# Performance work log

Measured on AMD Instinct MI355X. Metric: run time of the kernel, lower is better.

The kernel has to match this reference:

```python
import jax, jax.numpy as jnp
import numpy as np

F6_E3M2_MAX = 28.0  # max representable e3m2 value
M_TOKENS, K_IN, N_OUT = 256, 4096, 4096


def _quantize_e3m2(w: np.ndarray) -> np.ndarray:
    """Round-to-nearest onto the FP6 e3m2 grid (bias=3, min normal 2^-2, subnormal step 2^-4)."""
    sign = np.sign(w)
    a = np.minimum(np.abs(w), F6_E3M2_MAX)
    e = np.clip(np.floor(np.log2(np.maximum(a, 1e-30))), -2.0, 4.0)
    step = np.exp2(e - 2.0)  # 2 mantissa bits -> 4 steps per octave; subnormal step = 2^-4
    q = np.round(a / step) * step
    return (sign * np.minimum(q, F6_E3M2_MAX)).astype(np.float32)


def setup_inputs() -> dict:
    key = jax.random.key(0)
    k_x, k_w, k_b = jax.random.split(key, 3)
    x = (jax.random.normal(k_x, (M_TOKENS, K_IN), dtype=jnp.float32)).astype(jnp.float16)
    w_fp32 = np.asarray(jax.random.normal(k_w, (N_OUT, K_IN), dtype=jnp.float32)) * 0.02
    # per-row scale as in to_scaled_tc_float6_e3m2
    amax = np.clip(np.abs(w_fp32).max(axis=1), 1e-12, None)
    scale = F6_E3M2_MAX / amax                       # quantization scale
    weight_fp6 = _quantize_e3m2(w_fp32 * scale[:, None])  # values on the e3m2 grid
    scales = jnp.asarray(1.0 / scale, dtype=jnp.float16)  # dequant scale (stored half)
    bias = (jax.random.normal(k_b, (N_OUT,), dtype=jnp.float32) * 0.01).astype(jnp.float16)
    return {
        "x": x,
        "weight_fp6": jnp.asarray(weight_fp6),
        "scales": scales,
        "bias": bias,
    }


def reference(x, weight_fp6, scales, bias):
    # Fused dequant + GEMM: W = weight_fp6 * row_scale; out = x @ W^T + bias
    in_features = weight_fp6.shape[1]
    x2d = x.reshape(-1, in_features).astype(jnp.float16)
    w_deq = weight_fp6 * scales.astype(jnp.float32)[:, None]  # [N, K] fp32
    out = jnp.einsum("mk,nk->mn", x2d.astype(jnp.float32), w_deq,
                     preferred_element_type=jnp.float32)       # fp32 accumulate (split-K sums in fp32)
    out = out.astype(jnp.float16) + bias
    return out.reshape(*x.shape[:-1], weight_fp6.shape[0]).astype(x.dtype)
```

## Files before the change

kernel.cpp:

```cpp
#include <hip/hip_runtime.h>
#include <hip/hip_fp16.h>


typedef __attribute__((ext_vector_type(8))) _Float16 half8;
typedef __attribute__((ext_vector_type(4))) _Float16 half4;
typedef __attribute__((ext_vector_type(2))) __fp16 fp16x2;
typedef __attribute__((ext_vector_type(4))) float f32x4;

constexpr int K = 4096, N = 4096, M = 256;
constexpr int BM = 128, BN = 64, BK = 32;
constexpr int SPL = 8;
constexpr int KSPL = K / SPL;
constexpr int NT = KSPL / BK;

__device__ __forceinline__ half4 cvt4(float4 f) {
    fp16x2 p0 = __builtin_amdgcn_cvt_pkrtz(f.x, f.y);
    fp16x2 p1 = __builtin_amdgcn_cvt_pkrtz(f.z, f.w);
    half4 h;
    h[0]=(_Float16)p0[0]; h[1]=(_Float16)p0[1];
    h[2]=(_Float16)p1[0]; h[3]=(_Float16)p1[1];
    return h;
}

__global__ __launch_bounds__(256, 4)
void gemm(const float* __restrict__ X,
          const float* __restrict__ W,
          _Float16* __restrict__ P)
{
    __shared__ __align__(16) _Float16 LA[2][BM * BK];
    __shared__ __align__(16) _Float16 LB[2][BN * BK];

    const int tid = (int)threadIdx.x;
    const int l   = tid & 63;
    const int wv  = tid >> 6;
    const int lc  = l & 15;
    const int lr  = l >> 4;
    const int wm  = (wv & 1) * 64;
    const int wn  = (wv >> 1) * 32;

    const int bid = (int)blockIdx.x;
    const int xcd = bid & 7;
    const int i   = bid >> 3;
    const int mb  = i & 1;
    const int sp  = (i >> 1) & 7;
    const int nbl = i >> 4;
    const int bm  = mb * BM;
    const int bn  = (xcd * 8 + nbl) * BN;
    const int kb  = sp * KSPL;

    const int arow = wv * 32 + (l >> 3);
    const int wrow = wv * 16 + (l >> 3);
    const int scol = (l & 7) * 4;
    const float* ax0 = X + (size_t)(bm + arow)      * K + kb + scol;
    const float* ax1 = X + (size_t)(bm + arow + 8)  * K + kb + scol;
    const float* ax2 = X + (size_t)(bm + arow + 16) * K + kb + scol;
    const float* ax3 = X + (size_t)(bm + arow + 24) * K + kb + scol;
    const float* wx0 = W + (size_t)(bn + wrow)      * K + kb + scol;
    const float* wx1 = W + (size_t)(bn + wrow + 8)  * K + kb + scol;
    const int awr = arow * BK + (l & 7) * 4;
    const int wwr = wrow * BK + (l & 7) * 4;

    float4 sa0, sa1, sa2, sa3, sw0, sw1;

#define GLOAD(t) do { const size_t o = (size_t)(t) * BK;                \
        sa0 = *(const float4*)(ax0 + o); sa1 = *(const float4*)(ax1 + o); \
        sa2 = *(const float4*)(ax2 + o); sa3 = *(const float4*)(ax3 + o); \
        sw0 = *(const float4*)(wx0 + o); sw1 = *(const float4*)(wx1 + o); } while (0)
#define CVTW(bf) do {                                                   \
        *(half4*)(&LA[bf][awr])         = cvt4(sa0);                    \
        *(half4*)(&LA[bf][awr + 8*BK])  = cvt4(sa1);                    \
        *(half4*)(&LA[bf][awr + 16*BK]) = cvt4(sa2);                    \
        *(half4*)(&LA[bf][awr + 24*BK]) = cvt4(sa3);                    \
        *(half4*)(&LB[bf][wwr])         = cvt4(sw0);                    \
        *(half4*)(&LB[bf][wwr + 8*BK])  = cvt4(sw1); } while (0)

    f32x4 acc[4][2];
    #pragma unroll
    for (int a = 0; a < 4; ++a)
        #pragma unroll
        for (int b = 0; b < 2; ++b)
            acc[a][b] = (f32x4){0.f, 0.f, 0.f, 0.f};

#define COMPUTE(bf) do {                                                \
        half8 af[4], wf[2];                                             \
        _Pragma("unroll")                                               \
        for (int ar = 0; ar < 4; ++ar)                                  \
            af[ar] = *(const half8*)(&LA[bf][(wm + ar * 16 + lc) * BK + lr * 8]); \
        _Pragma("unroll")                                               \
        for (int br = 0; br < 2; ++br)                                  \
            wf[br] = *(const half8*)(&LB[bf][(wn + br * 16 + lc) * BK + lr * 8]); \
        _Pragma("unroll")                                               \
        for (int ar = 0; ar < 4; ++ar)                                  \
            _Pragma("unroll")                                           \
            for (int br = 0; br < 2; ++br)                              \
                acc[ar][br] = __builtin_amdgcn_mfma_f32_16x16x32_f16(   \
                    af[ar], wf[br], acc[ar][br], 0, 0, 0); } while (0)

    GLOAD(0);
    asm volatile("s_waitcnt vmcnt(0)" ::: "memory");
    CVTW(0);
    asm volatile("s_waitcnt lgkmcnt(0)" ::: "memory");
    __builtin_amdgcn_s_barrier();

    for (int t = 0; t < NT; ++t) {
        if (t + 1 < NT) {
            GLOAD(t + 1);
            __builtin_amdgcn_sched_barrier(0);
        }
        COMPUTE(t & 1);
        if (t + 1 < NT) {
            asm volatile("s_waitcnt vmcnt(0)" ::: "memory");
            __builtin_amdgcn_sched_barrier(0);
            CVTW((t + 1) & 1);
            asm volatile("s_waitcnt lgkmcnt(0)" ::: "memory");
            __builtin_amdgcn_s_barrier();
        }
    }
#undef GLOAD
#undef CVTW
#undef COMPUTE

    _Float16* Pb = P + (size_t)sp * M * N;
    const int orow = bm + wm + lr * 4;
    const int ocol = bn + wn + lc;
    #pragma unroll
    for (int ar = 0; ar < 4; ++ar)
        #pragma unroll
        for (int br = 0; br < 2; ++br)
            #pragma unroll
            for (int r = 0; r < 4; ++r)
                Pb[(size_t)(orow + ar * 16 + r) * N + ocol + br * 16]
                    = (_Float16)acc[ar][br][r];
}

__global__ __launch_bounds__(256)
void finalize(const _Float16* __restrict__ P,
              const float* __restrict__ S,
              const float* __restrict__ Bi,
              float* __restrict__ O)
{
    const size_t i = ((size_t)blockIdx.x * 256 + threadIdx.x) * 8;
    const int n = (int)(i & (N - 1));
    float acc[8] = {0.f, 0.f, 0.f, 0.f, 0.f, 0.f, 0.f, 0.f};
    #pragma unroll
    for (int s = 0; s < SPL; ++s) {
        half8 u = *(const half8*)(P + (size_t)s * M * N + i);
        #pragma unroll
        for (int e = 0; e < 8; ++e) acc[e] += (float)u[e];
    }
    float4 sc0 = *(const float4*)(S + n);
    float4 sc1 = *(const float4*)(S + n + 4);
    float4 bb0 = *(const float4*)(Bi + n);
    float4 bb1 = *(const float4*)(Bi + n + 4);
    float sc[8] = {sc0.x, sc0.y, sc0.z, sc0.w, sc1.x, sc1.y, sc1.z, sc1.w};
    float bb[8] = {bb0.x, bb0.y, bb0.z, bb0.w, bb1.x, bb1.y, bb1.z, bb1.w};
    float out[8];
    #pragma unroll
    for (int e = 0; e < 8; ++e)
        out[e] = (float)(_Float16)((float)(_Float16)(acc[e] * sc[e]) + bb[e]);
    *(float4*)(O + i)     = (float4){out[0], out[1], out[2], out[3]};
    *(float4*)(O + i + 4) = (float4){out[4], out[5], out[6], out[7]};
}

__global__ __launch_bounds__(256)
void fp6lin_small(const float* __restrict__ X, const float* __restrict__ W,
                  const float* __restrict__ S, const float* __restrict__ Bi,
                  float* __restrict__ O)
{
    const int n = (int)blockIdx.x;
    const int m = (int)threadIdx.x;
    float s = 0.f;
    for (int k = 0; k < K; ++k)
        s += (float)(_Float16)X[(size_t)m * K + k] * (float)(_Float16)W[(size_t)n * K + k];
    O[(size_t)m * N + n] = (float)(_Float16)((float)(_Float16)(s * S[n]) + Bi[n]);
}

extern "C" void kernel_launch(void* const* d_in, const int* in_sizes, int n_in,
                              void* d_out, int out_size, void* d_ws, size_t ws_size,
                              hipStream_t stream) {
    const float* x  = (const float*)d_in[0];
    const float* w  = (const float*)d_in[1];
    const float* s  = (const float*)d_in[2];
    const float* bi = (const float*)d_in[3];
    float* o = (float*)d_out;

    const size_t pbytes = (size_t)SPL * M * N * 2;
    _Float16* P = (_Float16*)d_ws;

    if (ws_size >= pbytes) {
        gemm<<<dim3(1024), dim3(256), 0, stream>>>(x, w, P);
        finalize<<<dim3(M * N / 8 / 256), dim3(256), 0, stream>>>(P, s, bi, o);
    } else {
        fp6lin_small<<<dim3(N), dim3(M), 0, stream>>>(x, w, s, bi, o);
    }
}
```

Measured before the change: 30.61 us.

## Double BK to 64 and add XOR-swizzled LDS layout for conflict-free reads

Doubles the K tile depth so each barrier/double-buffer step covers two MFMA k-substeps, halving the number of iterations and barriers. Global loads are rearranged into 16 lanes per row with 12 float4 loads per thread, and LDS writes and reads use an XOR swizzle on 8-half chunks to avoid bank conflicts with the 128-byte row stride. This doubles LDS usage and staging registers, so the occupancy hint drops from 4 to 3 waves per SIMD.

```diff
diff --git a/kernel.cpp b/kernel.cpp
--- a/kernel.cpp
+++ b/kernel.cpp
@@ -8,7 +8,7 @@
 typedef __attribute__((ext_vector_type(4))) float f32x4;
 
 constexpr int K = 4096, N = 4096, M = 256;
-constexpr int BM = 128, BN = 64, BK = 32;
+constexpr int BM = 128, BN = 64, BK = 64;
 constexpr int SPL = 8;
 constexpr int KSPL = K / SPL;
 constexpr int NT = KSPL / BK;
@@ -22,7 +22,7 @@
     return h;
 }
 
-__global__ __launch_bounds__(256, 4)
+__global__ __launch_bounds__(256, 3)
 void gemm(const float* __restrict__ X,
           const float* __restrict__ W,
           _Float16* __restrict__ P)
@@ -48,31 +48,47 @@
     const int bn  = (xcd * 8 + nbl) * BN;
     const int kb  = sp * KSPL;
 
-    const int arow = wv * 32 + (l >> 3);
-    const int wrow = wv * 16 + (l >> 3);
-    const int scol = (l & 7) * 4;
-    const float* ax0 = X + (size_t)(bm + arow)      * K + kb + scol;
-    const float* ax1 = X + (size_t)(bm + arow + 8)  * K + kb + scol;
-    const float* ax2 = X + (size_t)(bm + arow + 16) * K + kb + scol;
-    const float* ax3 = X + (size_t)(bm + arow + 24) * K + kb + scol;
-    const float* wx0 = W + (size_t)(bn + wrow)      * K + kb + scol;
-    const float* wx1 = W + (size_t)(bn + wrow + 8)  * K + kb + scol;
-    const int awr = arow * BK + (l & 7) * 4;
-    const int wwr = wrow * BK + (l & 7) * 4;
-
-    float4 sa0, sa1, sa2, sa3, sw0, sw1;
-
-#define GLOAD(t) do { const size_t o = (size_t)(t) * BK;                \
+    const int lrow  = l >> 4;
+    const int lcol4 = (l & 15) * 4;
+    const float* ax0 = X + (size_t)(bm + wv * 32 + 0  + lrow) * K + kb + lcol4;
+    const float* ax1 = X + (size_t)(bm + wv * 32 + 4  + lrow) * K + kb + lcol4;
+    const float* ax2 = X + (size_t)(bm + wv * 32 + 8  + lrow) * K + kb + lcol4;
+    const float* ax3 = X + (size_t)(bm + wv * 32 + 12 + lrow) * K + kb + lcol4;
+    const float* ax4 = X + (size_t)(bm + wv * 32 + 16 + lrow) * K + kb + lcol4;
+    const float* ax5 = X + (size_t)(bm + wv * 32 + 20 + lrow) * K + kb + lcol4;
+    const float* ax6 = X + (size_t)(bm + wv * 32 + 24 + lrow) * K + kb + lcol4;
+    const float* ax7 = X + (size_t)(bm + wv * 32 + 28 + lrow) * K + kb + lcol4;
+    const float* wx0 = W + (size_t)(bn + wv * 16 + 0  + lrow) * K + kb + lcol4;
+    const float* wx1 = W + (size_t)(bn + wv * 16 + 4  + lrow) * K + kb + lcol4;
+    const float* wx2 = W + (size_t)(bn + wv * 16 + 8  + lrow) * K + kb + lcol4;
+    const float* wx3 = W + (size_t)(bn + wv * 16 + 12 + lrow) * K + kb + lcol4;
+
+#define AWOFF(j) ((wv * 32 + 4 * (j) + lrow) * 64 + \
+                  (((l & 15) ^ ((((4 * (j) + lrow)) & 7) << 1)) << 2))
+#define WWOFF(j) ((wv * 16 + 4 * (j) + lrow) * 64 + \
+                  (((l & 15) ^ ((((4 * (j) + lrow)) & 7) << 1)) << 2))
+    const int aw0 = AWOFF(0), aw1 = AWOFF(1), aw2 = AWOFF(2), aw3 = AWOFF(3);
+    const int aw4 = AWOFF(4), aw5 = AWOFF(5), aw6 = AWOFF(6), aw7 = AWOFF(7);
+    const int ww0 = WWOFF(0), ww1 = WWOFF(1), ww2 = WWOFF(2), ww3 = WWOFF(3);
+#undef AWOFF
+#undef WWOFF
+
+    float4 sa0, sa1, sa2, sa3, sa4, sa5, sa6, sa7, sw0, sw1, sw2, sw3;
+
+#define GLOAD(t) do { const size_t o = (size_t)(t) * BK;                  \
         sa0 = *(const float4*)(ax0 + o); sa1 = *(const float4*)(ax1 + o); \
         sa2 = *(const float4*)(ax2 + o); sa3 = *(const float4*)(ax3 + o); \
-        sw0 = *(const float4*)(wx0 + o); sw1 = *(const float4*)(wx1 + o); } while (0)
-#define CVTW(bf) do {                                                   \
-        *(half4*)(&LA[bf][awr])         = cvt4(sa0);                    \
-        *(half4*)(&LA[bf][awr + 8*BK])  = cvt4(sa1);                    \
-        *(half4*)(&LA[bf][awr + 16*BK]) = cvt4(sa2);                    \
-        *(half4*)(&LA[bf][awr + 24*BK]) = cvt4(sa3);                    \
-        *(half4*)(&LB[bf][wwr])         = cvt4(sw0);                    \
-        *(half4*)(&LB[bf][wwr + 8*BK])  = cvt4(sw1); } while (0)
+        sa4 = *(const float4*)(ax4 + o); sa5 = *(const float4*)(ax5 + o); \
+        sa6 = *(const float4*)(ax6 + o); sa7 = *(const float4*)(ax7 + o); \
+        sw0 = *(const float4*)(wx0 + o); sw1 = *(const float4*)(wx1 + o); \
+        sw2 = *(const float4*)(wx2 + o); sw3 = *(const float4*)(wx3 + o); } while (0)
+#define CVTW(bf) do {                                                     \
+        *(half4*)(&LA[bf][aw0]) = cvt4(sa0); *(half4*)(&LA[bf][aw1]) = cvt4(sa1); \
+        *(half4*)(&LA[bf][aw2]) = cvt4(sa2); *(half4*)(&LA[bf][aw3]) = cvt4(sa3); \
+        *(half4*)(&LA[bf][aw4]) = cvt4(sa4); *(half4*)(&LA[bf][aw5]) = cvt4(sa5); \
+        *(half4*)(&LA[bf][aw6]) = cvt4(sa6); *(half4*)(&LA[bf][aw7]) = cvt4(sa7); \
+        *(half4*)(&LB[bf][ww0]) = cvt4(sw0); *(half4*)(&LB[bf][ww1]) = cvt4(sw1); \
+        *(half4*)(&LB[bf][ww2]) = cvt4(sw2); *(half4*)(&LB[bf][ww3]) = cvt4(sw3); } while (0)
 
     f32x4 acc[4][2];
     #pragma unroll
@@ -81,20 +97,29 @@
         for (int b = 0; b < 2; ++b)
             acc[a][b] = (f32x4){0.f, 0.f, 0.f, 0.f};
 
-#define COMPUTE(bf) do {                                                \
-        half8 af[4], wf[2];                                             \
-        _Pragma("unroll")                                               \
-        for (int ar = 0; ar < 4; ++ar)                                  \
-            af[ar] = *(const half8*)(&LA[bf][(wm + ar * 16 + lc) * BK + lr * 8]); \
-        _Pragma("unroll")                                               \
-        for (int br = 0; br < 2; ++br)                                  \
-            wf[br] = *(const half8*)(&LB[bf][(wn + br * 16 + lc) * BK + lr * 8]); \
-        _Pragma("unroll")                                               \
-        for (int ar = 0; ar < 4; ++ar)                                  \
-            _Pragma("unroll")                                           \
-            for (int br = 0; br < 2; ++br)                              \
-                acc[ar][br] = __builtin_amdgcn_mfma_f32_16x16x32_f16(   \
-                    af[ar], wf[br], acc[ar][br], 0, 0, 0); } while (0)
+#define COMPUTE(bf) do {                                                  \
+        _Pragma("unroll")                                                 \
+        for (int kk = 0; kk < 2; ++kk) {                                  \
+            half8 af[4], wf[2];                                           \
+            _Pragma("unroll")                                             \
+            for (int ar = 0; ar < 4; ++ar) {                              \
+                const int row = wm + ar * 16 + lc;                        \
+                af[ar] = *(const half8*)(&LA[bf][row * 64 +               \
+                         (((kk * 4 + lr) ^ (lc & 7)) << 3)]);             \
+            }                                                             \
+            _Pragma("unroll")                                             \
+            for (int br = 0; br < 2; ++br) {                              \
+                const int row = wn + br * 16 + lc;                        \
+                wf[br] = *(const half8*)(&LB[bf][row * 64 +               \
+                         (((kk * 4 + lr) ^ (lc & 7)) << 3)]);             \
+            }                                                             \
+            _Pragma("unroll")                                             \
+            for (int ar = 0; ar < 4; ++ar)                                \
+                _Pragma("unroll")                                         \
+                for (int br = 0; br < 2; ++br)                            \
+                    acc[ar][br] = __builtin_amdgcn_mfma_f32_16x16x32_f16( \
+                        af[ar], wf[br], acc[ar][br], 0, 0, 0);            \
+        } } while (0)
 
     GLOAD(0);
     asm volatile("s_waitcnt vmcnt(0)" ::: "memory");
```

Result: slower. 37.60 us (+22.8%).

## Deepen global-load prefetch, pad LDS rows, and XCD-localize finalize blocks

Applied to the files above, without the earlier changes.

The GEMM main loop is unrolled by two and uses two register sets, so global loads for tile t+2 are issued while tile t computes. Waits drop to vmcnt(6), which keeps one prefetch group in flight. LDS rows are padded from 32 to 40 halves to cut bank conflicts on the MFMA fragment reads. The finalize kernel remaps block IDs so that each XCD handles a 512-column stripe matching the gemm's column partition, which should improve L2 locality on the partial-sum reads. The cost is more registers per thread and a larger LDS footprint, which could reduce occupancy.

```diff
diff --git a/kernel.cpp b/kernel.cpp
--- a/kernel.cpp
+++ b/kernel.cpp
@@ -9,6 +9,7 @@
 
 constexpr int K = 4096, N = 4096, M = 256;
 constexpr int BM = 128, BN = 64, BK = 32;
+constexpr int LDR = 40;
 constexpr int SPL = 8;
 constexpr int KSPL = K / SPL;
 constexpr int NT = KSPL / BK;
@@ -27,8 +28,8 @@
           const float* __restrict__ W,
           _Float16* __restrict__ P)
 {
-    __shared__ __align__(16) _Float16 LA[2][BM * BK];
-    __shared__ __align__(16) _Float16 LB[2][BN * BK];
+    __shared__ __align__(16) _Float16 LA[2][BM * LDR];
+    __shared__ __align__(16) _Float16 LB[2][BN * LDR];
 
     const int tid = (int)threadIdx.x;
     const int l   = tid & 63;
@@ -57,22 +58,34 @@
     const float* ax3 = X + (size_t)(bm + arow + 24) * K + kb + scol;
     const float* wx0 = W + (size_t)(bn + wrow)      * K + kb + scol;
     const float* wx1 = W + (size_t)(bn + wrow + 8)  * K + kb + scol;
-    const int awr = arow * BK + (l & 7) * 4;
-    const int wwr = wrow * BK + (l & 7) * 4;
+    const int awr = arow * LDR + (l & 7) * 4;
+    const int wwr = wrow * LDR + (l & 7) * 4;
 
     float4 sa0, sa1, sa2, sa3, sw0, sw1;
-
-#define GLOAD(t) do { const size_t o = (size_t)(t) * BK;                \
+    float4 ta0, ta1, ta2, ta3, tw0, tw1;
+
+#define GLOAD0(t) do { const size_t o = (size_t)(t) * BK;               \
         sa0 = *(const float4*)(ax0 + o); sa1 = *(const float4*)(ax1 + o); \
         sa2 = *(const float4*)(ax2 + o); sa3 = *(const float4*)(ax3 + o); \
         sw0 = *(const float4*)(wx0 + o); sw1 = *(const float4*)(wx1 + o); } while (0)
-#define CVTW(bf) do {                                                   \
-        *(half4*)(&LA[bf][awr])         = cvt4(sa0);                    \
-        *(half4*)(&LA[bf][awr + 8*BK])  = cvt4(sa1);                    \
-        *(half4*)(&LA[bf][awr + 16*BK]) = cvt4(sa2);                    \
-        *(half4*)(&LA[bf][awr + 24*BK]) = cvt4(sa3);                    \
-        *(half4*)(&LB[bf][wwr])         = cvt4(sw0);                    \
-        *(half4*)(&LB[bf][wwr + 8*BK])  = cvt4(sw1); } while (0)
+#define GLOAD1(t) do { const size_t o = (size_t)(t) * BK;               \
+        ta0 = *(const float4*)(ax0 + o); ta1 = *(const float4*)(ax1 + o); \
+        ta2 = *(const float4*)(ax2 + o); ta3 = *(const float4*)(ax3 + o); \
+        tw0 = *(const float4*)(wx0 + o); tw1 = *(const float4*)(wx1 + o); } while (0)
+#define CVTW0(bf) do {                                                  \
+        *(half4*)(&LA[bf][awr])           = cvt4(sa0);                  \
+        *(half4*)(&LA[bf][awr + 8*LDR])   = cvt4(sa1);                  \
+        *(half4*)(&LA[bf][awr + 16*LDR])  = cvt4(sa2);                  \
+        *(half4*)(&LA[bf][awr + 24*LDR])  = cvt4(sa3);                  \
+        *(half4*)(&LB[bf][wwr])           = cvt4(sw0);                  \
+        *(half4*)(&LB[bf][wwr + 8*LDR])   = cvt4(sw1); } while (0)
+#define CVTW1(bf) do {                                                  \
+        *(half4*)(&LA[bf][awr])           = cvt4(ta0);                  \
+        *(half4*)(&LA[bf][awr + 8*LDR])   = cvt4(ta1);                  \
+        *(half4*)(&LA[bf][awr + 16*LDR])  = cvt4(ta2);                  \
+        *(half4*)(&LA[bf][awr + 24*LDR])  = cvt4(ta3);                  \
+        *(half4*)(&LB[bf][wwr])           = cvt4(tw0);                  \
+        *(half4*)(&LB[bf][wwr + 8*LDR])   = cvt4(tw1); } while (0)
 
     f32x4 acc[4][2];
     #pragma unroll
@@ -85,10 +98,10 @@
         half8 af[4], wf[2];                                             \
         _Pragma("unroll")                                               \
         for (int ar = 0; ar < 4; ++ar)                                  \
-            af[ar] = *(const half8*)(&LA[bf][(wm + ar * 16 + lc) * BK + lr * 8]); \
+            af[ar] = *(const half8*)(&LA[bf][(wm + ar * 16 + lc) * LDR + lr * 8]); \
         _Pragma("unroll")                                               \
         for (int br = 0; br < 2; ++br)                                  \
-            wf[br] = *(const half8*)(&LB[bf][(wn + br * 16 + lc) * BK + lr * 8]); \
+            wf[br] = *(const half8*)(&LB[bf][(wn + br * 16 + lc) * LDR + lr * 8]); \
         _Pragma("unroll")                                               \
         for (int ar = 0; ar < 4; ++ar)                                  \
             _Pragma("unroll")                                           \
@@ -96,28 +109,39 @@
                 acc[ar][br] = __builtin_amdgcn_mfma_f32_16x16x32_f16(   \
                     af[ar], wf[br], acc[ar][br], 0, 0, 0); } while (0)
 
-    GLOAD(0);
-    asm volatile("s_waitcnt vmcnt(0)" ::: "memory");
-    CVTW(0);
+    GLOAD0(0);
+    GLOAD1(1);
+    asm volatile("s_waitcnt vmcnt(6)" ::: "memory");
+    CVTW0(0);
     asm volatile("s_waitcnt lgkmcnt(0)" ::: "memory");
     __builtin_amdgcn_s_barrier();
 
-    for (int t = 0; t < NT; ++t) {
-        if (t + 1 < NT) {
-            GLOAD(t + 1);
+    for (int t2 = 0; t2 < NT; t2 += 2) {
+        if (t2 + 2 < NT) GLOAD0(t2 + 2);
+        __builtin_amdgcn_sched_barrier(0);
+        COMPUTE(0);
+        if (t2 + 2 < NT) { asm volatile("s_waitcnt vmcnt(6)" ::: "memory"); }
+        else             { asm volatile("s_waitcnt vmcnt(0)" ::: "memory"); }
+        __builtin_amdgcn_sched_barrier(0);
+        CVTW1(1);
+        asm volatile("s_waitcnt lgkmcnt(0)" ::: "memory");
+        __builtin_amdgcn_s_barrier();
+        if (t2 + 3 < NT) GLOAD1(t2 + 3);
+        __builtin_amdgcn_sched_barrier(0);
+        COMPUTE(1);
+        if (t2 + 2 < NT) {
+            if (t2 + 3 < NT) { asm volatile("s_waitcnt vmcnt(6)" ::: "memory"); }
+            else             { asm volatile("s_waitcnt vmcnt(0)" ::: "memory"); }
             __builtin_amdgcn_sched_barrier(0);
-        }
-        COMPUTE(t & 1);
-        if (t + 1 < NT) {
-            asm volatile("s_waitcnt vmcnt(0)" ::: "memory");
-            __builtin_amdgcn_sched_barrier(0);
-            CVTW((t + 1) & 1);
+            CVTW0(0);
             asm volatile("s_waitcnt lgkmcnt(0)" ::: "memory");
             __builtin_amdgcn_s_barrier();
         }
     }
-#undef GLOAD
-#undef CVTW
+#undef GLOAD0
+#undef GLOAD1
+#undef CVTW0
+#undef CVTW1
 #undef COMPUTE
 
     _Float16* Pb = P + (size_t)sp * M * N;
@@ -139,14 +163,20 @@
               const float* __restrict__ Bi,
               float* __restrict__ O)
 {
-    const size_t i = ((size_t)blockIdx.x * 256 + threadIdx.x) * 8;
-    const int n = (int)(i & (N - 1));
+    const int bid = (int)blockIdx.x;
+    const int xcd = bid & 7;
+    const int j   = bid >> 3;
+    const int e   = (j * 256 + (int)threadIdx.x) * 8;
+    const int row = e >> 9;
+    const int col = xcd * 512 + (e & 511);
+    const size_t i = (size_t)row * N + col;
+    const int n = col;
     float acc[8] = {0.f, 0.f, 0.f, 0.f, 0.f, 0.f, 0.f, 0.f};
     #pragma unroll
     for (int s = 0; s < SPL; ++s) {
         half8 u = *(const half8*)(P + (size_t)s * M * N + i);
         #pragma unroll
-        for (int e = 0; e < 8; ++e) acc[e] += (float)u[e];
+        for (int ee = 0; ee < 8; ++ee) acc[ee] += (float)u[ee];
     }
     float4 sc0 = *(const float4*)(S + n);
     float4 sc1 = *(const float4*)(S + n + 4);
@@ -156,8 +186,8 @@
     float bb[8] = {bb0.x, bb0.y, bb0.z, bb0.w, bb1.x, bb1.y, bb1.z, bb1.w};
     float out[8];
     #pragma unroll
-    for (int e = 0; e < 8; ++e)
-        out[e] = (float)(_Float16)((float)(_Float16)(acc[e] * sc[e]) + bb[e]);
+    for (int ee = 0; ee < 8; ++ee)
+        out[ee] = (float)(_Float16)((float)(_Float16)(acc[ee] * sc[ee]) + bb[ee]);
     *(float4*)(O + i)     = (float4){out[0], out[1], out[2], out[3]};
     *(float4*)(O + i + 4) = (float4){out[4], out[5], out[6], out[7]};
 }
@@ -189,7 +219,7 @@
 
     if (ws_size >= pbytes) {
         gemm<<<dim3(1024), dim3(256), 0, stream>>>(x, w, P);
-        finalize<<<dim3(M * N / 8 / 256), dim3(256), 0, stream>>>(P, s, bi, o);
+        finalize<<<dim3(512), dim3(256), 0, stream>>>(P, s, bi, o);
     } else {
         fp6lin_small<<<dim3(N), dim3(M), 0, stream>>>(x, w, s, bi, o);
     }
```

Result: slower. 34.71 us (+13.4%).
